# Optimization experiments

Hardware: AMD Instinct MI355X
Metric: run time of the kernel (lower is better)

The kernel has to match this reference:

```python
import jax, jax.numpy as jnp
import numpy as np

N_NODES = 50000
N_RAND_EDGES = 800000
N_GRAPHS = 64
IN_DIM, HID, HEADS = 1024, 64, 4
NEG_SLOPE = 0.2  # PyG GATConv default


def setup_inputs() -> dict:
    key = jax.random.key(0)
    ks = jax.random.split(key, 16)
    x = jax.random.normal(ks[0], (N_NODES, IN_DIM), dtype=jnp.float32)
    src = jax.random.randint(ks[1], (N_RAND_EDGES,), 0, N_NODES, dtype=jnp.int32)
    dst = jax.random.randint(ks[2], (N_RAND_EDGES,), 0, N_NODES, dtype=jnp.int32)
    loop = jnp.arange(N_NODES, dtype=jnp.int32)
    # PyG GATConv adds self-loops by default; bake them into edge_index.
    edge_index = jnp.stack([jnp.concatenate([src, loop]), jnp.concatenate([dst, loop])])
    batch = jnp.sort(jax.random.randint(ks[3], (N_NODES,), 0, N_GRAPHS, dtype=jnp.int32))
    s = 0.05
    W1 = jax.random.normal(ks[4], (IN_DIM, HEADS * HID), dtype=jnp.float32) * s
    att_src1 = jax.random.normal(ks[5], (HEADS, HID), dtype=jnp.float32) * s
    att_dst1 = jax.random.normal(ks[6], (HEADS, HID), dtype=jnp.float32) * s
    b1 = jnp.zeros((HEADS * HID,), dtype=jnp.float32)
    W2 = jax.random.normal(ks[7], (HEADS * HID, HID), dtype=jnp.float32) * s
    att_src2 = jax.random.normal(ks[8], (1, HID), dtype=jnp.float32) * s
    att_dst2 = jax.random.normal(ks[9], (1, HID), dtype=jnp.float32) * s
    b2 = jnp.zeros((HID,), dtype=jnp.float32)
    fc_w = jax.random.normal(ks[10], (HID, 2), dtype=jnp.float32) * s
    fc_b = jnp.zeros((2,), dtype=jnp.float32)
    return {"x": x, "edge_index": edge_index, "batch": batch,
            "W1": W1, "att_src1": att_src1, "att_dst1": att_dst1, "b1": b1,
            "W2": W2, "att_src2": att_src2, "att_dst2": att_dst2, "b2": b2,
            "fc_w": fc_w, "fc_b": fc_b}


def gat_conv(x, src, dst, W, a_src, a_dst, b):
    """PyG GATConv (eval mode, concat=True). x:[N,Fin] -> [N, H*C]."""
    N = x.shape[0]
    H, C = a_src.shape
    h = (x @ W).reshape(N, H, C)                      # [N,H,C]
    al_s = jnp.einsum('nhc,hc->nh', h, a_src)         # [N,H]
    al_d = jnp.einsum('nhc,hc->nh', h, a_dst)
    e = jax.nn.leaky_relu(al_s[src] + al_d[dst], NEG_SLOPE)   # [E,H]
    # segment-softmax over edges grouped by destination node
    m = jax.ops.segment_max(e, dst, num_segments=N)           # [N,H]
    w = jnp.exp(e - m[dst])
    denom = jax.ops.segment_sum(w, dst, num_segments=N)
    alpha = w / denom[dst]                                    # [E,H]
    msg = h[src] * alpha[:, :, None]                          # [E,H,C]
    out = jax.ops.segment_sum(msg, dst, num_segments=N)       # [N,H,C]
    return out.reshape(N, H * C) + b


def reference(x, edge_index, batch, W1, att_src1, att_dst1, b1,
              W2, att_src2, att_dst2, b2, fc_w, fc_b):
    src, dst = edge_index[0], edge_index[1]
    # dropout is identity in eval mode
    h = jax.nn.elu(gat_conv(x, src, dst, W1, att_src1, att_dst1, b1))
    h = jax.nn.elu(gat_conv(h, src, dst, W2, att_src2, att_dst2, b2))
    # global mean pool over graphs
    sums = jax.ops.segment_sum(h, batch, num_segments=N_GRAPHS)          # [G,HID]
    cnt = jax.ops.segment_sum(jnp.ones((h.shape[0],), h.dtype), batch,
                              num_segments=N_GRAPHS)
    pooled = sums / jnp.maximum(cnt, 1.0)[:, None]
    return pooled @ fc_w + fc_b                                          # [G,2]
```

## Files before the change

kernel.cpp:

```cpp
#include <hip/hip_runtime.h>
#include <hip/hip_bf16.h>

#define NNODES   50000
#define NGRAPHS  64
#define INDIM    1024
#define HIDC     64
#define HEADS1   4
#define F1       (HEADS1*HIDC)
#define NEG_SLOPE 0.2f

#define WS_COUNTS   0
#define WS_ZEROLEN  50000
#define WS_INDPTR   54208
#define WS_CURSOR   104256
#define WS_CSRSRC   154304
#define WS_CSRDST   1004304
#define WS_BSUM     1854304
#define WS_ALS1     1854368
#define WS_ALD1     2054368
#define WS_ALS2     2254368
#define WS_ALD2     2304368
#define WS_BP       2354368
#define WS_BP2      2485440
#define WS_H1B      2493632
#define WS_X2B      8893632
#define WS_H2B      15293632
#define WS_HFIN     16893632

typedef __attribute__((ext_vector_type(8))) short bf16x8;
typedef __attribute__((ext_vector_type(4))) float f32x4;

__device__ __forceinline__ ushort f2bf(float f) {
    union { float f; uint u; } v; v.f = f;
    uint r = v.u + 0x7fff + ((v.u >> 16) & 1);
    return (ushort)(r >> 16);
}
__device__ __forceinline__ float bf2f(ushort u) {
    union { uint u; float f; } v; v.u = (uint)u << 16; return v.f;
}

__global__ void zero_kernel(float* p, int n) {
    int i = blockIdx.x * blockDim.x + threadIdx.x;
    if (i < n) p[i] = 0.0f;
}

__global__ void hist_kernel(const int* __restrict__ dst, int* __restrict__ counts, int E) {
    int i = blockIdx.x * blockDim.x + threadIdx.x;
    if (i < E) atomicAdd(&counts[dst[i]], 1);
}

__global__ __launch_bounds__(1024) void scan1_kernel(const int* __restrict__ counts,
                                                     int* __restrict__ indptr,
                                                     int* __restrict__ bsum, int N) {
    __shared__ int sm[1024];
    int b = blockIdx.x;
    int i = b * 1024 + (int)threadIdx.x;
    int v = (i < N) ? counts[i] : 0;
    sm[threadIdx.x] = v;
    __syncthreads();
    for (int off = 1; off < 1024; off <<= 1) {
        int t = (threadIdx.x >= (unsigned)off) ? sm[threadIdx.x - off] : 0;
        __syncthreads();
        sm[threadIdx.x] += t;
        __syncthreads();
    }
    if (i < N) indptr[i + 1] = sm[threadIdx.x];
    if (threadIdx.x == 1023) bsum[b] = sm[1023];
}

__global__ void scan2_kernel(int* __restrict__ bsum, int nb) {
    int lane = threadIdx.x;
    int v = (lane < nb) ? bsum[lane] : 0;
    int orig = v;
    #pragma unroll
    for (int off = 1; off < 64; off <<= 1) {
        int t = __shfl_up(v, off, 64);
        if (lane >= off) v += t;
    }
    if (lane < nb) bsum[lane] = v - orig;
}

__global__ __launch_bounds__(1024) void scan3_kernel(const int* __restrict__ counts,
                                                     int* __restrict__ indptr,
                                                     int* __restrict__ cursor,
                                                     const int* __restrict__ bsum, int N) {
    int i = blockIdx.x * 1024 + (int)threadIdx.x;
    if (i == 0) indptr[0] = 0;
    if (i < N) {
        int incl = indptr[i + 1] + bsum[blockIdx.x];
        indptr[i + 1] = incl;
        cursor[i] = incl - counts[i];
    }
}

__global__ void fill_kernel(const int* __restrict__ src, const int* __restrict__ dst,
                            int* __restrict__ cursor, int* __restrict__ csr_src,
                            int* __restrict__ csr_dst, int E) {
    int i = blockIdx.x * blockDim.x + threadIdx.x;
    if (i < E) {
        int d = dst[i];
        int pos = atomicAdd(&cursor[d], 1);
        csr_src[pos] = src[i];
        csr_dst[pos] = d;
    }
}

__global__ void pack_w1(const float* __restrict__ W, ushort* __restrict__ Bp) {
    int o = blockIdx.x * blockDim.x + threadIdx.x;
    int j = o & 7;
    int lane = (o >> 3) & 63;
    int kchunk = (o >> 9) & 31;
    int ntile = o >> 14;
    int k = kchunk * 32 + (lane >> 4) * 8 + j;
    int n = ntile * 16 + (lane & 15);
    Bp[o] = f2bf(W[k * 256 + n]);
}

__global__ void pack_w2(const float* __restrict__ W, ushort* __restrict__ Bp) {
    int o = blockIdx.x * blockDim.x + threadIdx.x;
    int j = o & 7;
    int lane = (o >> 3) & 63;
    int kchunk = (o >> 9) & 7;
    int ntile = o >> 12;
    int k = kchunk * 32 + (lane >> 4) * 8 + j;
    int n = ntile * 16 + (lane & 15);
    Bp[o] = f2bf(W[k * 64 + n]);
}

__global__ __launch_bounds__(256) void gemm1_mfma(const float* __restrict__ A,
                                                  const ushort* __restrict__ Bp,
                                                  ushort* __restrict__ C,
                                                  const float* __restrict__ asrc,
                                                  const float* __restrict__ adst,
                                                  float* __restrict__ als,
                                                  float* __restrict__ ald,
                                                  int M) {
    __shared__ __align__(16) ushort Atile[2][128 * 32];
    const int K = 1024, N = 256;
    int tid = threadIdx.x;
    int lane = tid & 63;
    int w = tid >> 6;
    int wm = w >> 1, wn = w & 1;
    int m0 = blockIdx.x * 128;
    int n0 = blockIdx.y * 128;

    const float* srow[4];
    int soff[4];
    #pragma unroll
    for (int l = 0; l < 4; ++l) {
        int slot = l * 256 + tid;
        int m = slot >> 3, hc = slot & 7;
        int c = hc >> 1;
        int row = m0 + m; if (row >= M) row = M - 1;
        srow[l] = A + (size_t)row * K + hc * 4;
        soff[l] = (m * 4 + (c ^ ((m >> 1) & 3))) * 8 + (hc & 1) * 4;
    }
    int afrag_off[4];
    #pragma unroll
    for (int mt = 0; mt < 4; ++mt) {
        int r = wm * 64 + mt * 16 + (lane & 15);
        int cq = lane >> 4;
        afrag_off[mt] = (r * 4 + (cq ^ ((r >> 1) & 3))) * 8;
    }
    const ushort* bbase[4];
    #pragma unroll
    for (int nt = 0; nt < 4; ++nt) {
        int ntile = blockIdx.y * 8 + wn * 4 + nt;
        bbase[nt] = Bp + ((size_t)(ntile * 32) * 64 + lane) * 8;
    }

    f32x4 acc[4][4] = {};
    float4 v[4];
    #pragma unroll
    for (int l = 0; l < 4; ++l) v[l] = *(const float4*)(srow[l]);

    for (int kc = 0; kc < 32; ++kc) {
        ushort* At = Atile[kc & 1];
        #pragma unroll
        for (int l = 0; l < 4; ++l) {
            ushort4 b;
            b.x = f2bf(v[l].x); b.y = f2bf(v[l].y);
            b.z = f2bf(v[l].z); b.w = f2bf(v[l].w);
            *(ushort4*)&At[soff[l]] = b;
        }
        if (kc < 31) {
            #pragma unroll
            for (int l = 0; l < 4; ++l)
                v[l] = *(const float4*)(srow[l] + (kc + 1) * 32);
        }
        bf16x8 bfr[4];
        #pragma unroll
        for (int nt = 0; nt < 4; ++nt)
            bfr[nt] = *(const bf16x8*)(bbase[nt] + (size_t)kc * 64 * 8);
        __syncthreads();
        bf16x8 afr[4];
        #pragma unroll
        for (int mt = 0; mt < 4; ++mt)
            afr[mt] = *(const bf16x8*)&At[afrag_off[mt]];
        #pragma unroll
        for (int mt = 0; mt < 4; ++mt)
            #pragma unroll
            for (int nt = 0; nt < 4; ++nt)
                acc[mt][nt] = __builtin_amdgcn_mfma_f32_16x16x32_bf16(afr[mt], bfr[nt], acc[mt][nt], 0, 0, 0);
    }

    int head = blockIdx.y * 2 + wn;
    float a_s[4], a_d[4];
    #pragma unroll
    for (int nt = 0; nt < 4; ++nt) {
        a_s[nt] = asrc[head * 64 + nt * 16 + (lane & 15)];
        a_d[nt] = adst[head * 64 + nt * 16 + (lane & 15)];
    }
    #pragma unroll
    for (int mt = 0; mt < 4; ++mt) {
        #pragma unroll
        for (int nt = 0; nt < 4; ++nt) {
            int col = n0 + wn * 64 + nt * 16 + (lane & 15);
            #pragma unroll
            for (int r = 0; r < 4; ++r) {
                int row = m0 + wm * 64 + mt * 16 + (lane >> 4) * 4 + r;
                if (row < M) C[(size_t)row * N + col] = f2bf(acc[mt][nt][r]);
            }
        }
        #pragma unroll
        for (int r = 0; r < 4; ++r) {
            int row = m0 + wm * 64 + mt * 16 + (lane >> 4) * 4 + r;
            float s = 0.f, d = 0.f;
            #pragma unroll
            for (int nt = 0; nt < 4; ++nt) {
                float c = acc[mt][nt][r];
                s = fmaf(c, a_s[nt], s);
                d = fmaf(c, a_d[nt], d);
            }
            #pragma unroll
            for (int off = 1; off < 16; off <<= 1) {
                s += __shfl_xor(s, off, 64);
                d += __shfl_xor(d, off, 64);
            }
            if ((lane & 15) == 0 && row < M) {
                als[row * 4 + head] = s;
                ald[row * 4 + head] = d;
            }
        }
    }
}

__global__ __launch_bounds__(256) void gemm2_mfma(const ushort* __restrict__ Ab,
                                                  const ushort* __restrict__ Bp,
                                                  ushort* __restrict__ C,
                                                  const float* __restrict__ asrc,
                                                  const float* __restrict__ adst,
                                                  float* __restrict__ als,
                                                  float* __restrict__ ald,
                                                  int M) {
    int tid = threadIdx.x;
    int lane = tid & 63;
    int w = tid >> 6;
    int m0 = blockIdx.x * 128 + w * 32;

    f32x4 acc[2][4] = {};
    #pragma unroll 2
    for (int kc = 0; kc < 8; ++kc) {
        bf16x8 afr[2];
        #pragma unroll
        for (int mt = 0; mt < 2; ++mt) {
            int r = m0 + mt * 16 + (lane & 15);
            if (r >= M) r = M - 1;
            afr[mt] = *(const bf16x8*)&Ab[(size_t)r * 256 + kc * 32 + (lane >> 4) * 8];
        }
        #pragma unroll
        for (int nt = 0; nt < 4; ++nt) {
            bf16x8 bfr = *(const bf16x8*)&Bp[((nt * 8 + kc) * 64 + lane) * 8];
            acc[0][nt] = __builtin_amdgcn_mfma_f32_16x16x32_bf16(afr[0], bfr, acc[0][nt], 0, 0, 0);
            acc[1][nt] = __builtin_amdgcn_mfma_f32_16x16x32_bf16(afr[1], bfr, acc[1][nt], 0, 0, 0);
        }
    }
    float a_s[4], a_d[4];
    #pragma unroll
    for (int nt = 0; nt < 4; ++nt) {
        a_s[nt] = asrc[nt * 16 + (lane & 15)];
        a_d[nt] = adst[nt * 16 + (lane & 15)];
    }
    #pragma unroll
    for (int mt = 0; mt < 2; ++mt) {
        #pragma unroll
        for (int nt = 0; nt < 4; ++nt) {
            int col = nt * 16 + (lane & 15);
            #pragma unroll
            for (int r = 0; r < 4; ++r) {
                int row = m0 + mt * 16 + (lane >> 4) * 4 + r;
                if (row < M) C[(size_t)row * 64 + col] = f2bf(acc[mt][nt][r]);
            }
        }
        #pragma unroll
        for (int r = 0; r < 4; ++r) {
            int row = m0 + mt * 16 + (lane >> 4) * 4 + r;
            float s = 0.f, d = 0.f;
            #pragma unroll
            for (int nt = 0; nt < 4; ++nt) {
                float c = acc[mt][nt][r];
                s = fmaf(c, a_s[nt], s);
                d = fmaf(c, a_d[nt], d);
            }
            #pragma unroll
            for (int off = 1; off < 16; off <<= 1) {
                s += __shfl_xor(s, off, 64);
                d += __shfl_xor(d, off, 64);
            }
            if ((lane & 15) == 0 && row < M) {
                als[row] = s;
                ald[row] = d;
            }
        }
    }
}

__device__ __forceinline__ float wave_reduce_sum(float v) {
    #pragma unroll
    for (int off = 32; off > 0; off >>= 1) v += __shfl_xor(v, off, 64);
    return v;
}

__device__ __forceinline__ float edge_w(float e) {
    e = (e > 0.f) ? e : NEG_SLOPE * e;
    return __expf(e);
}

__global__ __launch_bounds__(256) void agg1_kernel(const ushort* __restrict__ h,
                                                   const float* __restrict__ als,
                                                   const float* __restrict__ ald,
                                                   const int* __restrict__ indptr,
                                                   const int* __restrict__ csr_src,
                                                   const float* __restrict__ bias,
                                                   ushort* __restrict__ out, int N) {
    __shared__ float4 lacc[4][64];
    __shared__ float  lden[4][64];
    int n = blockIdx.x;
    int lane = threadIdx.x & 63;
    int wv = threadIdx.x >> 6;
    int hd = lane >> 4;
    int beg = indptr[n], end = indptr[n + 1];
    float ald_h = ald[n * 4 + hd];
    float4 acc = make_float4(0.f, 0.f, 0.f, 0.f);
    float den = 0.f;
    int p = beg + wv;
    for (; p + 4 < end; p += 8) {
        int s0 = csr_src[p], s1 = csr_src[p + 4];
        float w0 = edge_w(als[s0 * 4 + hd] + ald_h);
        float w1 = edge_w(als[s1 * 4 + hd] + ald_h);
        ushort4 a0 = *(const ushort4*)&h[(size_t)s0 * 256 + lane * 4];
        ushort4 a1 = *(const ushort4*)&h[(size_t)s1 * 256 + lane * 4];
        acc.x = fmaf(w0, bf2f(a0.x), fmaf(w1, bf2f(a1.x), acc.x));
        acc.y = fmaf(w0, bf2f(a0.y), fmaf(w1, bf2f(a1.y), acc.y));
        acc.z = fmaf(w0, bf2f(a0.z), fmaf(w1, bf2f(a1.z), acc.z));
        acc.w = fmaf(w0, bf2f(a0.w), fmaf(w1, bf2f(a1.w), acc.w));
        den += w0 + w1;
    }
    if (p < end) {
        int s0 = csr_src[p];
        float w0 = edge_w(als[s0 * 4 + hd] + ald_h);
        ushort4 a0 = *(const ushort4*)&h[(size_t)s0 * 256 + lane * 4];
        acc.x = fmaf(w0, bf2f(a0.x), acc.x);
        acc.y = fmaf(w0, bf2f(a0.y), acc.y);
        acc.z = fmaf(w0, bf2f(a0.z), acc.z);
        acc.w = fmaf(w0, bf2f(a0.w), acc.w);
        den += w0;
    }
    lacc[wv][lane] = acc;
    lden[wv][lane] = den;
    __syncthreads();
    if (wv == 0) {
        float4 a = lacc[0][lane];
        float4 a1 = lacc[1][lane], a2 = lacc[2][lane], a3 = lacc[3][lane];
        a.x += a1.x + a2.x + a3.x;
        a.y += a1.y + a2.y + a3.y;
        a.z += a1.z + a2.z + a3.z;
        a.w += a1.w + a2.w + a3.w;
        float d = lden[0][lane] + lden[1][lane] + lden[2][lane] + lden[3][lane];
        float4 bv = *(const float4*)&bias[lane * 4];
        float inv = 1.0f / d;
        float o0 = a.x * inv + bv.x, o1 = a.y * inv + bv.y;
        float o2 = a.z * inv + bv.z, o3 = a.w * inv + bv.w;
        o0 = (o0 > 0.f) ? o0 : (__expf(o0) - 1.0f);
        o1 = (o1 > 0.f) ? o1 : (__expf(o1) - 1.0f);
        o2 = (o2 > 0.f) ? o2 : (__expf(o2) - 1.0f);
        o3 = (o3 > 0.f) ? o3 : (__expf(o3) - 1.0f);
        ushort4 ob; ob.x = f2bf(o0); ob.y = f2bf(o1); ob.z = f2bf(o2); ob.w = f2bf(o3);
        *(ushort4*)&out[(size_t)n * 256 + lane * 4] = ob;
    }
}

__global__ __launch_bounds__(256) void agg2_kernel(const ushort* __restrict__ h,
                                                   const float* __restrict__ als,
                                                   const float* __restrict__ ald,
                                                   const int* __restrict__ indptr,
                                                   const int* __restrict__ csr_src,
                                                   const float* __restrict__ bias,
                                                   float* __restrict__ out, int N) {
    __shared__ float2 lacc[8][32];
    __shared__ float  lden[8][32];
    int n = blockIdx.x;
    int lane = threadIdx.x & 63;
    int wv = threadIdx.x >> 6;
    int sl = wv * 2 + (lane >> 5);
    int l32 = lane & 31;
    int beg = indptr[n], end = indptr[n + 1];
    float ald_n = ald[n];
    float2 acc = make_float2(0.f, 0.f);
    float den = 0.f;
    for (int p = beg + sl; p < end; p += 8) {
        int s = csr_src[p];
        float wt = edge_w(als[s] + ald_n);
        ushort2 hv = *(const ushort2*)&h[(size_t)s * 64 + l32 * 2];
        acc.x = fmaf(wt, bf2f(hv.x), acc.x);
        acc.y = fmaf(wt, bf2f(hv.y), acc.y);
        den += wt;
    }
    lacc[sl][l32] = acc;
    lden[sl][l32] = den;
    __syncthreads();
    if (threadIdx.x < 32) {
        int c = threadIdx.x;
        float2 a = make_float2(0.f, 0.f);
        float d = 0.f;
        #pragma unroll
        for (int s = 0; s < 8; ++s) {
            a.x += lacc[s][c].x; a.y += lacc[s][c].y;
            d += lden[s][c];
        }
        float inv = 1.0f / d;
        float o0 = a.x * inv + bias[c * 2];
        float o1 = a.y * inv + bias[c * 2 + 1];
        o0 = (o0 > 0.f) ? o0 : (__expf(o0) - 1.0f);
        o1 = (o1 > 0.f) ? o1 : (__expf(o1) - 1.0f);
        *(float2*)&out[(size_t)n * 64 + c * 2] = make_float2(o0, o1);
    }
}

__global__ __launch_bounds__(256) void pool_fc_kernel(const float* __restrict__ hfin,
                                                      const int* __restrict__ batch,
                                                      const float* __restrict__ fc_w,
                                                      const float* __restrict__ fc_b,
                                                      float* __restrict__ out, int N) {
    __shared__ float lacc[4][64];
    int g = blockIdx.x;
    int beg, end;
    {
        int lo = 0, hi = N;
        while (lo < hi) { int mid = (lo + hi) >> 1; if (batch[mid] < g) lo = mid + 1; else hi = mid; }
        beg = lo;
        lo = beg; hi = N;
        while (lo < hi) { int mid = (lo + hi) >> 1; if (batch[mid] < g + 1) lo = mid + 1; else hi = mid; }
        end = lo;
    }
    int lane = threadIdx.x & 63;
    int wv = threadIdx.x >> 6;
    float acc = 0.f;
    for (int n = beg + wv; n < end; n += 4)
        acc += hfin[(size_t)n * 64 + lane];
    lacc[wv][lane] = acc;
    __syncthreads();
    if (wv == 0) {
        float s = lacc[0][lane] + lacc[1][lane] + lacc[2][lane] + lacc[3][lane];
        float cnt = fmaxf((float)(end - beg), 1.0f);
        float pooled = s / cnt;
        float p0 = wave_reduce_sum(pooled * fc_w[lane * 2 + 0]);
        float p1 = wave_reduce_sum(pooled * fc_w[lane * 2 + 1]);
        if (lane == 0) {
            out[g * 2 + 0] = p0 + fc_b[0];
            out[g * 2 + 1] = p1 + fc_b[1];
        }
    }
}

extern "C" void kernel_launch(void* const* d_in, const int* in_sizes, int n_in,
                              void* d_out, int out_size, void* d_ws, size_t ws_size,
                              hipStream_t stream) {
    const float* x      = (const float*)d_in[0];
    const int*   ei     = (const int*)d_in[1];
    const int*   batch  = (const int*)d_in[2];
    const float* W1     = (const float*)d_in[3];
    const float* asrc1  = (const float*)d_in[4];
    const float* adst1  = (const float*)d_in[5];
    const float* b1     = (const float*)d_in[6];
    const float* W2     = (const float*)d_in[7];
    const float* asrc2  = (const float*)d_in[8];
    const float* adst2  = (const float*)d_in[9];
    const float* b2     = (const float*)d_in[10];
    const float* fc_w   = (const float*)d_in[11];
    const float* fc_b   = (const float*)d_in[12];
    float* out          = (float*)d_out;

    const int N = in_sizes[2];
    const int E = in_sizes[1] / 2;
    const int* src = ei;
    const int* dst = ei + E;

    float* ws = (float*)d_ws;
    int*    counts  = (int*)(ws + WS_COUNTS);
    int*    indptr  = (int*)(ws + WS_INDPTR);
    int*    cursor  = (int*)(ws + WS_CURSOR);
    int*    csr_src = (int*)(ws + WS_CSRSRC);
    int*    csr_dst = (int*)(ws + WS_CSRDST);
    int*    bsum    = (int*)(ws + WS_BSUM);
    float*  al_s1   = ws + WS_ALS1;
    float*  al_d1   = ws + WS_ALD1;
    float*  al_s2   = ws + WS_ALS2;
    float*  al_d2   = ws + WS_ALD2;
    ushort* bp      = (ushort*)(ws + WS_BP);
    ushort* bp2     = (ushort*)(ws + WS_BP2);
    ushort* h1b     = (ushort*)(ws + WS_H1B);
    ushort* x2b     = (ushort*)(ws + WS_X2B);
    ushort* h2b     = (ushort*)(ws + WS_H2B);
    float*  hfin    = ws + WS_HFIN;

    const int nb = (N + 1023) / 1024;

    zero_kernel<<<(WS_ZEROLEN + 255) / 256, 256, 0, stream>>>(ws, WS_ZEROLEN);
    pack_w1<<<(INDIM * F1) / 256, 256, 0, stream>>>(W1, bp);
    pack_w2<<<(F1 * HIDC) / 256, 256, 0, stream>>>(W2, bp2);
    hist_kernel<<<(E + 255) / 256, 256, 0, stream>>>(dst, counts, E);
    scan1_kernel<<<nb, 1024, 0, stream>>>(counts, indptr, bsum, N);
    scan2_kernel<<<1, 64, 0, stream>>>(bsum, nb);
    scan3_kernel<<<nb, 1024, 0, stream>>>(counts, indptr, cursor, bsum, N);
    fill_kernel<<<(E + 255) / 256, 256, 0, stream>>>(src, dst, cursor, csr_src, csr_dst, E);
    gemm1_mfma<<<dim3((N + 127) / 128, F1 / 128), 256, 0, stream>>>(
        x, bp, h1b, asrc1, adst1, al_s1, al_d1, N);
    agg1_kernel<<<N, 256, 0, stream>>>(h1b, al_s1, al_d1, indptr, csr_src, b1, x2b, N);
    gemm2_mfma<<<(N + 127) / 128, 256, 0, stream>>>(
        x2b, bp2, h2b, asrc2, adst2, al_s2, al_d2, N);
    agg2_kernel<<<N, 256, 0, stream>>>(h2b, al_s2, al_d2, indptr, csr_src, b2, hfin, N);
    pool_fc_kernel<<<NGRAPHS, 256, 0, stream>>>(hfin, batch, fc_w, fc_b, out, N);
}
```

Baseline: 668.1 us.

## Widen gemm1 block tile to full 256 columns so x is read once

The first-layer GEMM now has each block compute all 256 output columns (each wave 128 columns, 8 N-tiles) instead of splitting N across two grid columns. The fp32 input x, which dominates memory traffic, is loaded and converted to bf16 once instead of twice. B-fragment loads move inside the N loop and the barrier moves before the next prefetch. In exchange, accumulators double to 128 floats per lane, which raises register pressure and lowers occupancy, and the grid has half as many blocks.

New measurement: 647.7 us. 3.1% less time.

```diff
diff --git a/kernel.cpp b/kernel.cpp
--- a/kernel.cpp
+++ b/kernel.cpp
@@ -142,7 +142,6 @@
     int w = tid >> 6;
     int wm = w >> 1, wn = w & 1;
     int m0 = blockIdx.x * 128;
-    int n0 = blockIdx.y * 128;
 
     const float* srow[4];
     int soff[4];
@@ -162,14 +161,14 @@
         int cq = lane >> 4;
         afrag_off[mt] = (r * 4 + (cq ^ ((r >> 1) & 3))) * 8;
     }
-    const ushort* bbase[4];
-    #pragma unroll
-    for (int nt = 0; nt < 4; ++nt) {
-        int ntile = blockIdx.y * 8 + wn * 4 + nt;
+    const ushort* bbase[8];
+    #pragma unroll
+    for (int nt = 0; nt < 8; ++nt) {
+        int ntile = wn * 8 + nt;
         bbase[nt] = Bp + ((size_t)(ntile * 32) * 64 + lane) * 8;
     }
 
-    f32x4 acc[4][4] = {};
+    f32x4 acc[4][8] = {};
     float4 v[4];
     #pragma unroll
     for (int l = 0; l < 4; ++l) v[l] = *(const float4*)(srow[l]);
@@ -183,39 +182,37 @@
             b.z = f2bf(v[l].z); b.w = f2bf(v[l].w);
             *(ushort4*)&At[soff[l]] = b;
         }
+        __syncthreads();
         if (kc < 31) {
             #pragma unroll
             for (int l = 0; l < 4; ++l)
                 v[l] = *(const float4*)(srow[l] + (kc + 1) * 32);
         }
-        bf16x8 bfr[4];
-        #pragma unroll
-        for (int nt = 0; nt < 4; ++nt)
-            bfr[nt] = *(const bf16x8*)(bbase[nt] + (size_t)kc * 64 * 8);
-        __syncthreads();
         bf16x8 afr[4];
         #pragma unroll
         for (int mt = 0; mt < 4; ++mt)
             afr[mt] = *(const bf16x8*)&At[afrag_off[mt]];
         #pragma unroll
-        for (int mt = 0; mt < 4; ++mt)
-            #pragma unroll
-            for (int nt = 0; nt < 4; ++nt)
-                acc[mt][nt] = __builtin_amdgcn_mfma_f32_16x16x32_bf16(afr[mt], bfr[nt], acc[mt][nt], 0, 0, 0);
-    }
-
-    int head = blockIdx.y * 2 + wn;
-    float a_s[4], a_d[4];
-    #pragma unroll
-    for (int nt = 0; nt < 4; ++nt) {
-        a_s[nt] = asrc[head * 64 + nt * 16 + (lane & 15)];
-        a_d[nt] = adst[head * 64 + nt * 16 + (lane & 15)];
+        for (int nt = 0; nt < 8; ++nt) {
+            bf16x8 bfr = *(const bf16x8*)(bbase[nt] + (size_t)kc * 64 * 8);
+            #pragma unroll
+            for (int mt = 0; mt < 4; ++mt)
+                acc[mt][nt] = __builtin_amdgcn_mfma_f32_16x16x32_bf16(afr[mt], bfr, acc[mt][nt], 0, 0, 0);
+        }
+    }
+
+    float a_s[8], a_d[8];
+    #pragma unroll
+    for (int nt = 0; nt < 8; ++nt) {
+        int col = wn * 128 + nt * 16 + (lane & 15);
+        a_s[nt] = asrc[col];
+        a_d[nt] = adst[col];
     }
     #pragma unroll
     for (int mt = 0; mt < 4; ++mt) {
         #pragma unroll
-        for (int nt = 0; nt < 4; ++nt) {
-            int col = n0 + wn * 64 + nt * 16 + (lane & 15);
+        for (int nt = 0; nt < 8; ++nt) {
+            int col = wn * 128 + nt * 16 + (lane & 15);
             #pragma unroll
             for (int r = 0; r < 4; ++r) {
                 int row = m0 + wm * 64 + mt * 16 + (lane >> 4) * 4 + r;
@@ -223,23 +220,27 @@
             }
         }
         #pragma unroll
-        for (int r = 0; r < 4; ++r) {
-            int row = m0 + wm * 64 + mt * 16 + (lane >> 4) * 4 + r;
-            float s = 0.f, d = 0.f;
-            #pragma unroll
-            for (int nt = 0; nt < 4; ++nt) {
-                float c = acc[mt][nt][r];
-                s = fmaf(c, a_s[nt], s);
-                d = fmaf(c, a_d[nt], d);
-            }
-            #pragma unroll
-            for (int off = 1; off < 16; off <<= 1) {
-                s += __shfl_xor(s, off, 64);
-                d += __shfl_xor(d, off, 64);
-            }
-            if ((lane & 15) == 0 && row < M) {
-                als[row * 4 + head] = s;
-                ald[row * 4 + head] = d;
+        for (int hg = 0; hg < 2; ++hg) {
+            int head = wn * 2 + hg;
+            #pragma unroll
+            for (int r = 0; r < 4; ++r) {
+                int row = m0 + wm * 64 + mt * 16 + (lane >> 4) * 4 + r;
+                float s = 0.f, d = 0.f;
+                #pragma unroll
+                for (int q = 0; q < 4; ++q) {
+                    float c = acc[mt][4 * hg + q][r];
+                    s = fmaf(c, a_s[4 * hg + q], s);
+                    d = fmaf(c, a_d[4 * hg + q], d);
+                }
+                #pragma unroll
+                for (int off = 1; off < 16; off <<= 1) {
+                    s += __shfl_xor(s, off, 64);
+                    d += __shfl_xor(d, off, 64);
+                }
+                if ((lane & 15) == 0 && row < M) {
+                    als[row * 4 + head] = s;
+                    ald[row * 4 + head] = d;
+                }
             }
         }
     }
@@ -524,7 +525,7 @@
     scan2_kernel<<<1, 64, 0, stream>>>(bsum, nb);
     scan3_kernel<<<nb, 1024, 0, stream>>>(counts, indptr, cursor, bsum, N);
     fill_kernel<<<(E + 255) / 256, 256, 0, stream>>>(src, dst, cursor, csr_src, csr_dst, E);
-    gemm1_mfma<<<dim3((N + 127) / 128, F1 / 128), 256, 0, stream>>>(
+    gemm1_mfma<<<(N + 127) / 128, 256, 0, stream>>>(
         x, bp, h1b, asrc1, adst1, al_s1, al_d1, N);
     agg1_kernel<<<N, 256, 0, stream>>>(h1b, al_s1, al_d1, indptr, csr_src, b1, x2b, N);
     gemm2_mfma<<<(N + 127) / 128, 256, 0, stream>>>(
```
